# Optimization experiments

Measured on AMD Instinct MI355X. Metric: run time of the kernel, lower is better.

## Reference

```python
import jax, jax.numpy as jnp
import numpy as np

DIM = 1024
HID = 2816
E = 8
TOPK = 2
B, S = 4, 1024


def setup_inputs() -> dict:
    key = jax.random.key(0)
    k_x, k_g, k1, k2, k3 = jax.random.split(key, 5)
    scale_d = 1.0 / np.sqrt(DIM)
    scale_h = 1.0 / np.sqrt(HID)
    return {
        "x": jax.random.normal(k_x, (B, S, DIM), dtype=jnp.float32),
        "Wg": jax.random.normal(k_g, (E, DIM), dtype=jnp.float32) * scale_d,   # gate: Linear(dim, E), no bias
        "W1": jax.random.normal(k1, (E, HID, DIM), dtype=jnp.float32) * scale_d,  # swiglu gate proj
        "W3": jax.random.normal(k3, (E, HID, DIM), dtype=jnp.float32) * scale_d,  # swiglu up proj
        "W2": jax.random.normal(k2, (E, DIM, HID), dtype=jnp.float32) * scale_h,  # down proj
    }


def reference(x, Wg, W1, W3, W2):
    Bsz, Ssz, D = x.shape
    xt = x.reshape(Bsz * Ssz, D)                        # [T, D]

    # Gating: top-k over expert scores, softmax over selected logits
    scores = xt @ Wg.T                                   # [T, E]
    top_vals, top_idx = jax.lax.top_k(scores, TOPK)      # [T, K]
    weights = jax.nn.softmax(top_vals, axis=-1)          # [T, K]

    # Dense grouped SwiGLU: run every expert on every token (vectorized),
    # then gather the top-k expert outputs per token.
    h1 = jnp.einsum('td,ehd->teh', xt, W1)               # [T, E, H]
    h3 = jnp.einsum('td,ehd->teh', xt, W3)               # [T, E, H]
    expert_out = jnp.einsum('teh,edh->ted', jax.nn.silu(h1) * h3, W2)  # [T, E, D]

    # Gather per-token selected experts and combine with gate weights
    idx = top_idx[:, :, None]                            # [T, K, 1]
    sel = jnp.take_along_axis(expert_out, idx, axis=1)   # [T, K, D]
    out = jnp.sum(sel * weights[:, :, None], axis=1)     # [T, D]
    return out.reshape(Bsz, Ssz, D)
```

## Files before the change

kernel.cpp:

```cpp
#include <hip/hip_runtime.h>
#include <hip/hip_bf16.h>

#define DIM  1024
#define HID  2816
#define NE   8
#define NTOK 4096
#define NPAIR 8192
#define CAP  8192

typedef __bf16 bf16x8 __attribute__((ext_vector_type(8)));
typedef float f32x4 __attribute__((ext_vector_type(4)));

#define OFF_CNT  0
#define OFF_LIST 1024
#define OFF_WP   (OFF_LIST + NE*CAP*4)
#define OFF_H1   (OFF_WP + NPAIR*4)
#define OFF_XB   ((size_t)1 << 20)
#define OFF_W1B  ((size_t)10 << 20)
#define OFF_W3B  ((size_t)57 << 20)
#define OFF_H2   ((size_t)106 << 20)
#define WS_NEED  (OFF_H2 + (size_t)NPAIR * HID * 2)

#define GLB(p) ((const __attribute__((address_space(1))) void*)(p))
#define LDS(p) ((__attribute__((address_space(3))) void*)(p))

__global__ __launch_bounds__(64) void gate_kernel(
    const float* __restrict__ x, const float* __restrict__ Wg,
    int* __restrict__ counts, int* __restrict__ list, float* __restrict__ wpair) {
  int t = blockIdx.x;
  int lane = threadIdx.x;
  const float* xp = x + (size_t)t * DIM;
  float xr[16];
#pragma unroll
  for (int i = 0; i < 16; ++i) xr[i] = xp[lane + 64 * i];
  float s[NE];
#pragma unroll
  for (int e = 0; e < NE; ++e) {
    const float* wp = Wg + e * DIM;
    float acc = 0.f;
#pragma unroll
    for (int i = 0; i < 16; ++i) acc += xr[i] * wp[lane + 64 * i];
#pragma unroll
    for (int off = 32; off >= 1; off >>= 1) acc += __shfl_xor(acc, off, 64);
    s[e] = acc;
  }
  if (lane == 0) {
    int i0 = 0; float b0 = s[0];
#pragma unroll
    for (int e = 1; e < NE; ++e) if (s[e] > b0) { b0 = s[e]; i0 = e; }
    int i1 = -1; float b1 = -1e30f;
#pragma unroll
    for (int e = 0; e < NE; ++e) if (e != i0 && s[e] > b1) { b1 = s[e]; i1 = e; }
    float e1 = __expf(b1 - b0);
    float w0 = 1.f / (1.f + e1);
    float w1 = e1 * w0;
    int s0 = atomicAdd(&counts[i0], 1);
    list[i0 * CAP + s0] = 2 * t;
    wpair[2 * t] = w0;
    int s1 = atomicAdd(&counts[i1], 1);
    list[i1 * CAP + s1] = 2 * t + 1;
    wpair[2 * t + 1] = w1;
  }
}

__global__ __launch_bounds__(256) void cvt_kernel(
    const float* __restrict__ src, __bf16* __restrict__ dst) {
  size_t i = (((size_t)blockIdx.x * 256) + threadIdx.x) * 8;
  float4 f0 = *(const float4*)(src + i);
  float4 f1 = *(const float4*)(src + i + 4);
  bf16x8 v;
  v[0] = (__bf16)f0.x; v[1] = (__bf16)f0.y; v[2] = (__bf16)f0.z; v[3] = (__bf16)f0.w;
  v[4] = (__bf16)f1.x; v[5] = (__bf16)f1.y; v[6] = (__bf16)f1.z; v[7] = (__bf16)f1.w;
  *(bf16x8*)(dst + i) = v;
}


__global__ __launch_bounds__(256, 2) void up2_kernel(
    const __bf16* __restrict__ xb, const __bf16* __restrict__ w1b,
    const __bf16* __restrict__ w3b, const int* __restrict__ counts,
    const int* __restrict__ list, __bf16* __restrict__ Hbuf) {
  int e = blockIdx.z;
  int cnt = counts[e];
  int m0 = blockIdx.y * 128;
  if (m0 >= cnt) return;
  int h0 = blockIdx.x * 128;

  __shared__ __bf16 As[128 * 64];
  __shared__ __bf16 B1s[128 * 64];
  __shared__ __bf16 B3s[128 * 64];

  int tid = threadIdx.x;
  int lane = tid & 63;
  int w = tid >> 6;
  int cl = lane & 15, hi = lane >> 4;
  int wr = w >> 1, wc = w & 1;
  int l8 = lane >> 3, cc = lane & 7;

  const __bf16* asrc[4];
  const __bf16* b1src[4];
  const __bf16* b3src[4];
#pragma unroll
  for (int i = 0; i < 4; ++i) {
    int r = (w * 4 + i) * 8 + l8;
    int csel = (cc ^ (r & 7)) * 8;
    int mrow = m0 + r; if (mrow > cnt - 1) mrow = cnt - 1;
    int p = list[e * CAP + mrow];
    asrc[i]  = xb + (size_t)(p >> 1) * DIM + csel;
    b1src[i] = w1b + ((size_t)e * HID + h0 + r) * DIM + csel;
    b3src[i] = w3b + ((size_t)e * HID + h0 + r) * DIM + csel;
  }

  f32x4 acc1[4][4] = {};
  f32x4 acc3[4][4] = {};

  for (int k0 = 0; k0 < DIM; k0 += 64) {
#pragma unroll
    for (int i = 0; i < 4; ++i) {
      int q = (w * 4 + i) * 1024;
      __builtin_amdgcn_global_load_lds(GLB(asrc[i] + k0),  LDS((char*)As  + q), 16, 0, 0);
      __builtin_amdgcn_global_load_lds(GLB(b1src[i] + k0), LDS((char*)B1s + q), 16, 0, 0);
      __builtin_amdgcn_global_load_lds(GLB(b3src[i] + k0), LDS((char*)B3s + q), 16, 0, 0);
    }
    __syncthreads();
#pragma unroll
    for (int ks = 0; ks < 2; ++ks) {
      bf16x8 a[4], bb1[4], bb3[4];
#pragma unroll
      for (int mi = 0; mi < 4; ++mi) {
        int r = wr * 64 + mi * 16 + cl;
        int c = (hi + ks * 4) ^ (cl & 7);
        a[mi] = *(const bf16x8*)((const char*)As + r * 128 + c * 16);
      }
#pragma unroll
      for (int ni = 0; ni < 4; ++ni) {
        int r = wc * 64 + ni * 16 + cl;
        int c = (hi + ks * 4) ^ (cl & 7);
        bb1[ni] = *(const bf16x8*)((const char*)B1s + r * 128 + c * 16);
        bb3[ni] = *(const bf16x8*)((const char*)B3s + r * 128 + c * 16);
      }
#pragma unroll
      for (int mi = 0; mi < 4; ++mi)
#pragma unroll
        for (int ni = 0; ni < 4; ++ni) {
          acc1[mi][ni] = __builtin_amdgcn_mfma_f32_16x16x32_bf16(a[mi], bb1[ni], acc1[mi][ni], 0, 0, 0);
          acc3[mi][ni] = __builtin_amdgcn_mfma_f32_16x16x32_bf16(a[mi], bb3[ni], acc3[mi][ni], 0, 0, 0);
        }
    }
    __syncthreads();
  }

#pragma unroll
  for (int mi = 0; mi < 4; ++mi) {
#pragma unroll
    for (int rr = 0; rr < 4; ++rr) {
      int m = m0 + wr * 64 + mi * 16 + hi * 4 + rr;
      if (m < cnt) {
        int p = list[e * CAP + m];
        __bf16* hp = Hbuf + (size_t)p * HID + h0 + wc * 64 + cl;
#pragma unroll
        for (int ni = 0; ni < 4; ++ni) {
          float v1 = acc1[mi][ni][rr], v3 = acc3[mi][ni][rr];
          float g = (v1 / (1.f + __expf(-v1))) * v3;
          hp[ni * 16] = (__bf16)g;
        }
      }
    }
  }
}

__global__ __launch_bounds__(256, 2) void down2_kernel(
    const __bf16* __restrict__ Hbuf, const __bf16* __restrict__ w2b,
    const int* __restrict__ counts, const int* __restrict__ list,
    const float* __restrict__ wpair, float* __restrict__ out) {
  int e = blockIdx.z;
  int cnt = counts[e];
  int m0 = blockIdx.y * 128;
  if (m0 >= cnt) return;
  int d0 = blockIdx.x * 128;

  __shared__ __bf16 As[128 * 64];
  __shared__ __bf16 Bs[128 * 64];

  int tid = threadIdx.x;
  int lane = tid & 63;
  int w = tid >> 6;
  int cl = lane & 15, hi = lane >> 4;
  int wr = w >> 1, wc = w & 1;
  int l8 = lane >> 3, cc = lane & 7;

  const __bf16* asrc[4];
  const __bf16* bsrc[4];
#pragma unroll
  for (int i = 0; i < 4; ++i) {
    int r = (w * 4 + i) * 8 + l8;
    int csel = (cc ^ (r & 7)) * 8;
    int mrow = m0 + r; if (mrow > cnt - 1) mrow = cnt - 1;
    int p = list[e * CAP + mrow];
    asrc[i] = Hbuf + (size_t)p * HID + csel;
    bsrc[i] = w2b + ((size_t)e * DIM + d0 + r) * HID + csel;
  }

  f32x4 acc[4][4] = {};

  for (int k0 = 0; k0 < HID; k0 += 64) {
#pragma unroll
    for (int i = 0; i < 4; ++i) {
      int q = (w * 4 + i) * 1024;
      __builtin_amdgcn_global_load_lds(GLB(asrc[i] + k0), LDS((char*)As + q), 16, 0, 0);
      __builtin_amdgcn_global_load_lds(GLB(bsrc[i] + k0), LDS((char*)Bs + q), 16, 0, 0);
    }
    __syncthreads();
#pragma unroll
    for (int ks = 0; ks < 2; ++ks) {
      bf16x8 a[4], b[4];
#pragma unroll
      for (int mi = 0; mi < 4; ++mi) {
        int r = wr * 64 + mi * 16 + cl;
        int c = (hi + ks * 4) ^ (cl & 7);
        a[mi] = *(const bf16x8*)((const char*)As + r * 128 + c * 16);
      }
#pragma unroll
      for (int ni = 0; ni < 4; ++ni) {
        int r = wc * 64 + ni * 16 + cl;
        int c = (hi + ks * 4) ^ (cl & 7);
        b[ni] = *(const bf16x8*)((const char*)Bs + r * 128 + c * 16);
      }
#pragma unroll
      for (int mi = 0; mi < 4; ++mi)
#pragma unroll
        for (int ni = 0; ni < 4; ++ni)
          acc[mi][ni] = __builtin_amdgcn_mfma_f32_16x16x32_bf16(a[mi], b[ni], acc[mi][ni], 0, 0, 0);
    }
    __syncthreads();
  }

#pragma unroll
  for (int mi = 0; mi < 4; ++mi) {
#pragma unroll
    for (int rr = 0; rr < 4; ++rr) {
      int m = m0 + wr * 64 + mi * 16 + hi * 4 + rr;
      if (m < cnt) {
        int p = list[e * CAP + m];
        int t = p >> 1;
        float wgt = wpair[p];
        float* op = out + (size_t)t * DIM + d0 + wc * 64 + cl;
#pragma unroll
        for (int ni = 0; ni < 4; ++ni)
          atomicAdd(&op[ni * 16], wgt * acc[mi][ni][rr]);
      }
    }
  }
}

__device__ __forceinline__ void cvt_store16(__bf16* dst, const float* src) {
#pragma unroll
  for (int j = 0; j < 2; ++j) {
    float4 f0 = *(const float4*)(src + j * 8);
    float4 f1 = *(const float4*)(src + j * 8 + 4);
    bf16x8 v;
    v[0] = (__bf16)f0.x; v[1] = (__bf16)f0.y; v[2] = (__bf16)f0.z; v[3] = (__bf16)f0.w;
    v[4] = (__bf16)f1.x; v[5] = (__bf16)f1.y; v[6] = (__bf16)f1.z; v[7] = (__bf16)f1.w;
    *(bf16x8*)(dst + j * 8) = v;
  }
}

__global__ __launch_bounds__(256) void up_kernel(
    const float* __restrict__ x, const float* __restrict__ W1,
    const float* __restrict__ W3, const int* __restrict__ counts,
    const int* __restrict__ list, __bf16* __restrict__ Hbuf) {
  int e = blockIdx.z;
  int cnt = counts[e];
  int m0 = blockIdx.y * 64;
  if (m0 >= cnt) return;
  int h0 = blockIdx.x * 64;

  __shared__ __bf16 As[64][72];
  __shared__ __bf16 B1s[64][72];
  __shared__ __bf16 B3s[64][72];

  int tid = threadIdx.x;
  int r = tid >> 2;
  int cs = (tid & 3) * 16;

  const float* asrc = nullptr;
  int mrow = m0 + r;
  if (mrow < cnt) {
    int p = list[e * CAP + mrow];
    asrc = x + (size_t)(p >> 1) * DIM;
  }
  const float* b1src = W1 + ((size_t)e * HID + (h0 + r)) * DIM;
  const float* b3src = W3 + ((size_t)e * HID + (h0 + r)) * DIM;

  int lane = tid & 63;
  int w = tid >> 6;
  int wr = w >> 1, wc = w & 1;
  int cl = lane & 15, hi = lane >> 4;

  f32x4 acc1[2][2] = {};
  f32x4 acc3[2][2] = {};

  for (int k0 = 0; k0 < DIM; k0 += 64) {
    if (asrc) {
      cvt_store16(&As[r][cs], asrc + k0 + cs);
    } else {
      bf16x8 z = {};
      *(bf16x8*)&As[r][cs] = z;
      *(bf16x8*)&As[r][cs + 8] = z;
    }
    cvt_store16(&B1s[r][cs], b1src + k0 + cs);
    cvt_store16(&B3s[r][cs], b3src + k0 + cs);
    __syncthreads();
#pragma unroll
    for (int ks = 0; ks < 64; ks += 32) {
      bf16x8 a[2], b1f[2], b3f[2];
#pragma unroll
      for (int mi = 0; mi < 2; ++mi)
        a[mi] = *(const bf16x8*)&As[wr * 32 + mi * 16 + cl][ks + hi * 8];
#pragma unroll
      for (int ni = 0; ni < 2; ++ni) {
        b1f[ni] = *(const bf16x8*)&B1s[wc * 32 + ni * 16 + cl][ks + hi * 8];
        b3f[ni] = *(const bf16x8*)&B3s[wc * 32 + ni * 16 + cl][ks + hi * 8];
      }
#pragma unroll
      for (int mi = 0; mi < 2; ++mi)
#pragma unroll
        for (int ni = 0; ni < 2; ++ni) {
          acc1[mi][ni] = __builtin_amdgcn_mfma_f32_16x16x32_bf16(a[mi], b1f[ni], acc1[mi][ni], 0, 0, 0);
          acc3[mi][ni] = __builtin_amdgcn_mfma_f32_16x16x32_bf16(a[mi], b3f[ni], acc3[mi][ni], 0, 0, 0);
        }
    }
    __syncthreads();
  }

#pragma unroll
  for (int mi = 0; mi < 2; ++mi) {
#pragma unroll
    for (int rr = 0; rr < 4; ++rr) {
      int m = m0 + wr * 32 + mi * 16 + hi * 4 + rr;
      if (m < cnt) {
        int p = list[e * CAP + m];
        __bf16* hp = Hbuf + (size_t)p * HID + h0 + wc * 32 + cl;
#pragma unroll
        for (int ni = 0; ni < 2; ++ni) {
          float v1 = acc1[mi][ni][rr], v3 = acc3[mi][ni][rr];
          float g = (v1 / (1.f + __expf(-v1))) * v3;
          hp[ni * 16] = (__bf16)g;
        }
      }
    }
  }
}

__global__ __launch_bounds__(256) void down_kernel(
    const __bf16* __restrict__ Hbuf, const float* __restrict__ W2,
    const int* __restrict__ counts, const int* __restrict__ list,
    const float* __restrict__ wpair, float* __restrict__ out) {
  int e = blockIdx.z;
  int cnt = counts[e];
  int m0 = blockIdx.y * 64;
  if (m0 >= cnt) return;
  int d0 = blockIdx.x * 64;

  __shared__ __bf16 As[64][72];
  __shared__ __bf16 Bs[64][72];

  int tid = threadIdx.x;
  int r = tid >> 2;
  int cs = (tid & 3) * 16;

  const __bf16* asrc = nullptr;
  int mrow = m0 + r;
  if (mrow < cnt) {
    int p = list[e * CAP + mrow];
    asrc = Hbuf + (size_t)p * HID;
  }
  const float* bsrc = W2 + ((size_t)e * DIM + (d0 + r)) * HID;

  int lane = tid & 63;
  int w = tid >> 6;
  int wr = w >> 1, wc = w & 1;
  int cl = lane & 15, hi = lane >> 4;

  f32x4 acc[2][2] = {};

  for (int k0 = 0; k0 < HID; k0 += 64) {
    if (asrc) {
      *(bf16x8*)&As[r][cs]     = *(const bf16x8*)(asrc + k0 + cs);
      *(bf16x8*)&As[r][cs + 8] = *(const bf16x8*)(asrc + k0 + cs + 8);
    } else {
      bf16x8 z = {};
      *(bf16x8*)&As[r][cs] = z;
      *(bf16x8*)&As[r][cs + 8] = z;
    }
    cvt_store16(&Bs[r][cs], bsrc + k0 + cs);
    __syncthreads();
#pragma unroll
    for (int ks = 0; ks < 64; ks += 32) {
      bf16x8 a[2], b[2];
#pragma unroll
      for (int mi = 0; mi < 2; ++mi)
        a[mi] = *(const bf16x8*)&As[wr * 32 + mi * 16 + cl][ks + hi * 8];
#pragma unroll
      for (int ni = 0; ni < 2; ++ni)
        b[ni] = *(const bf16x8*)&Bs[wc * 32 + ni * 16 + cl][ks + hi * 8];
#pragma unroll
      for (int mi = 0; mi < 2; ++mi)
#pragma unroll
        for (int ni = 0; ni < 2; ++ni)
          acc[mi][ni] = __builtin_amdgcn_mfma_f32_16x16x32_bf16(a[mi], b[ni], acc[mi][ni], 0, 0, 0);
    }
    __syncthreads();
  }

#pragma unroll
  for (int mi = 0; mi < 2; ++mi) {
#pragma unroll
    for (int rr = 0; rr < 4; ++rr) {
      int m = m0 + wr * 32 + mi * 16 + hi * 4 + rr;
      if (m < cnt) {
        int p = list[e * CAP + m];
        int t = p >> 1;
        float wgt = wpair[p];
        float* op = out + (size_t)t * DIM + d0 + wc * 32 + cl;
#pragma unroll
        for (int ni = 0; ni < 2; ++ni)
          atomicAdd(&op[ni * 16], wgt * acc[mi][ni][rr]);
      }
    }
  }
}

extern "C" void kernel_launch(void* const* d_in, const int* in_sizes, int n_in,
                              void* d_out, int out_size, void* d_ws, size_t ws_size,
                              hipStream_t stream) {
  const float* x  = (const float*)d_in[0];
  const float* Wg = (const float*)d_in[1];
  const float* W1 = (const float*)d_in[2];
  const float* W3 = (const float*)d_in[3];
  const float* W2 = (const float*)d_in[4];
  float* out = (float*)d_out;

  char* ws = (char*)d_ws;
  int* counts  = (int*)(ws + OFF_CNT);
  int* list    = (int*)(ws + OFF_LIST);
  float* wpair = (float*)(ws + OFF_WP);

  hipMemsetAsync(counts, 0, 64, stream);
  hipMemsetAsync(d_out, 0, (size_t)out_size * sizeof(float), stream);

  gate_kernel<<<NTOK, 64, 0, stream>>>(x, Wg, counts, list, wpair);

  if (ws_size >= WS_NEED) {
    __bf16* xb   = (__bf16*)(ws + OFF_XB);
    __bf16* w1b  = (__bf16*)(ws + OFF_W1B);
    __bf16* w3b  = (__bf16*)(ws + OFF_W3B);
    __bf16* Hbuf = (__bf16*)(ws + OFF_H2);

    cvt_kernel<<<NTOK * DIM / 2048, 256, 0, stream>>>(x, xb);
    cvt_kernel<<<NE * HID * DIM / 2048, 256, 0, stream>>>(W1, w1b);
    cvt_kernel<<<NE * HID * DIM / 2048, 256, 0, stream>>>(W3, w3b);

    up2_kernel<<<dim3(HID / 128, CAP / 128, NE), 256, 0, stream>>>(
        xb, w1b, w3b, counts, list, Hbuf);

    cvt_kernel<<<NE * DIM * HID / 2048, 256, 0, stream>>>(W2, w1b);

    down2_kernel<<<dim3(DIM / 128, CAP / 128, NE), 256, 0, stream>>>(
        Hbuf, w1b, counts, list, wpair, out);
  } else {
    __bf16* Hbuf = (__bf16*)(ws + OFF_H1);
    up_kernel<<<dim3(HID / 64, CAP / 64, NE), 256, 0, stream>>>(x, W1, W3, counts, list, Hbuf);
    down_kernel<<<dim3(DIM / 64, CAP / 64, NE), 256, 0, stream>>>(Hbuf, W2, counts, list, wpair, out);
  }
}
```

Before: 399.2 us.

## Double-buffer MoE GEMMs, enlarge up tile, replace atomics with combine pass

The up-projection kernel now uses 512 threads with 256-row tiles and a single packed B buffer holding the W1 and W3 rows. It applies the gate weight in its SwiGLU epilogue. Both GEMM kernels gain double-buffered LDS staging so the next K tile loads while the current one computes. The down kernel writes per-pair bf16 outputs to a scratch buffer instead of doing float atomicAdds into the output, and a new combine kernel sums each token's two rows, which also removes the output memset. This trades atomic contention for an extra pass and bf16 rounding of the partial outputs, and relies on every token having exactly two pair slots.

```diff
diff --git a/kernel.cpp b/kernel.cpp
--- a/kernel.cpp
+++ b/kernel.cpp
@@ -75,92 +75,96 @@
 }
 
 
-__global__ __launch_bounds__(256, 2) void up2_kernel(
+__global__ __launch_bounds__(512, 2) void up3_kernel(
     const __bf16* __restrict__ xb, const __bf16* __restrict__ w1b,
     const __bf16* __restrict__ w3b, const int* __restrict__ counts,
-    const int* __restrict__ list, __bf16* __restrict__ Hbuf) {
+    const int* __restrict__ list, const float* __restrict__ wpair,
+    __bf16* __restrict__ Hbuf) {
   int e = blockIdx.z;
   int cnt = counts[e];
-  int m0 = blockIdx.y * 128;
+  int m0 = blockIdx.y * 256;
   if (m0 >= cnt) return;
   int h0 = blockIdx.x * 128;
 
-  __shared__ __bf16 As[128 * 64];
-  __shared__ __bf16 B1s[128 * 64];
-  __shared__ __bf16 B3s[128 * 64];
+  __shared__ __bf16 As[2][256 * 64];
+  __shared__ __bf16 Bs[2][256 * 64];
 
   int tid = threadIdx.x;
   int lane = tid & 63;
   int w = tid >> 6;
+  int wr = w >> 2, wc = w & 3;
   int cl = lane & 15, hi = lane >> 4;
-  int wr = w >> 1, wc = w & 1;
   int l8 = lane >> 3, cc = lane & 7;
 
   const __bf16* asrc[4];
-  const __bf16* b1src[4];
-  const __bf16* b3src[4];
+  const __bf16* bsrc[4];
 #pragma unroll
   for (int i = 0; i < 4; ++i) {
-    int r = (w * 4 + i) * 8 + l8;
+    int r = i * 64 + w * 8 + l8;
     int csel = (cc ^ (r & 7)) * 8;
     int mrow = m0 + r; if (mrow > cnt - 1) mrow = cnt - 1;
     int p = list[e * CAP + mrow];
-    asrc[i]  = xb + (size_t)(p >> 1) * DIM + csel;
-    b1src[i] = w1b + ((size_t)e * HID + h0 + r) * DIM + csel;
-    b3src[i] = w3b + ((size_t)e * HID + h0 + r) * DIM + csel;
-  }
-
-  f32x4 acc1[4][4] = {};
-  f32x4 acc3[4][4] = {};
-
-  for (int k0 = 0; k0 < DIM; k0 += 64) {
-#pragma unroll
-    for (int i = 0; i < 4; ++i) {
-      int q = (w * 4 + i) * 1024;
-      __builtin_amdgcn_global_load_lds(GLB(asrc[i] + k0),  LDS((char*)As  + q), 16, 0, 0);
-      __builtin_amdgcn_global_load_lds(GLB(b1src[i] + k0), LDS((char*)B1s + q), 16, 0, 0);
-      __builtin_amdgcn_global_load_lds(GLB(b3src[i] + k0), LDS((char*)B3s + q), 16, 0, 0);
-    }
-    __syncthreads();
-#pragma unroll
-    for (int ks = 0; ks < 2; ++ks) {
-      bf16x8 a[4], bb1[4], bb3[4];
-#pragma unroll
-      for (int mi = 0; mi < 4; ++mi) {
-        int r = wr * 64 + mi * 16 + cl;
-        int c = (hi + ks * 4) ^ (cl & 7);
-        a[mi] = *(const bf16x8*)((const char*)As + r * 128 + c * 16);
-      }
-#pragma unroll
-      for (int ni = 0; ni < 4; ++ni) {
-        int r = wc * 64 + ni * 16 + cl;
-        int c = (hi + ks * 4) ^ (cl & 7);
-        bb1[ni] = *(const bf16x8*)((const char*)B1s + r * 128 + c * 16);
-        bb3[ni] = *(const bf16x8*)((const char*)B3s + r * 128 + c * 16);
-      }
-#pragma unroll
-      for (int mi = 0; mi < 4; ++mi)
-#pragma unroll
-        for (int ni = 0; ni < 4; ++ni) {
-          acc1[mi][ni] = __builtin_amdgcn_mfma_f32_16x16x32_bf16(a[mi], bb1[ni], acc1[mi][ni], 0, 0, 0);
-          acc3[mi][ni] = __builtin_amdgcn_mfma_f32_16x16x32_bf16(a[mi], bb3[ni], acc3[mi][ni], 0, 0, 0);
-        }
-    }
-    __syncthreads();
-  }
-
-#pragma unroll
-  for (int mi = 0; mi < 4; ++mi) {
+    asrc[i] = xb + (size_t)(p >> 1) * DIM + csel;
+    bsrc[i] = (r < 128 ? w1b + ((size_t)e * HID + h0 + r) * DIM
+                       : w3b + ((size_t)e * HID + h0 + (r - 128)) * DIM) + csel;
+  }
+
+  f32x4 acc1[8][2] = {};
+  f32x4 acc3[8][2] = {};
+
+#define UP_STAGE(buf, k0)                                                          \
+  _Pragma("unroll") for (int i = 0; i < 4; ++i) {                                  \
+    int q = i * 8192 + w * 1024;                                                   \
+    __builtin_amdgcn_global_load_lds(GLB(asrc[i] + (k0)), LDS((char*)As[buf] + q), 16, 0, 0); \
+    __builtin_amdgcn_global_load_lds(GLB(bsrc[i] + (k0)), LDS((char*)Bs[buf] + q), 16, 0, 0); \
+  }
+
+#define UP_COMPUTE(buf)                                                            \
+  _Pragma("unroll") for (int ks = 0; ks < 2; ++ks) {                               \
+    int c = hi + ks * 4;                                                           \
+    bf16x8 a[8], b1[2], b3[2];                                                     \
+    _Pragma("unroll") for (int mi = 0; mi < 8; ++mi) {                             \
+      int r = wr * 128 + mi * 16 + cl;                                             \
+      a[mi] = *(const bf16x8*)((const char*)As[buf] + r * 128 + ((c ^ (r & 7)) * 16)); \
+    }                                                                              \
+    _Pragma("unroll") for (int ni = 0; ni < 2; ++ni) {                             \
+      int r1 = wc * 32 + ni * 16 + cl;                                             \
+      b1[ni] = *(const bf16x8*)((const char*)Bs[buf] + r1 * 128 + ((c ^ (r1 & 7)) * 16)); \
+      int r3 = 128 + r1;                                                           \
+      b3[ni] = *(const bf16x8*)((const char*)Bs[buf] + r3 * 128 + ((c ^ (r3 & 7)) * 16)); \
+    }                                                                              \
+    _Pragma("unroll") for (int mi = 0; mi < 8; ++mi)                               \
+      _Pragma("unroll") for (int ni = 0; ni < 2; ++ni) {                           \
+        acc1[mi][ni] = __builtin_amdgcn_mfma_f32_16x16x32_bf16(a[mi], b1[ni], acc1[mi][ni], 0, 0, 0); \
+        acc3[mi][ni] = __builtin_amdgcn_mfma_f32_16x16x32_bf16(a[mi], b3[ni], acc3[mi][ni], 0, 0, 0); \
+      }                                                                            \
+  }
+
+  UP_STAGE(0, 0);
+  __syncthreads();
+  int cur = 0;
+#pragma unroll 1
+  for (int kt = 0; kt < DIM / 64 - 1; ++kt) {
+    UP_STAGE(cur ^ 1, (kt + 1) * 64);
+    UP_COMPUTE(cur);
+    __syncthreads();
+    cur ^= 1;
+  }
+  UP_COMPUTE(cur);
+
+#pragma unroll
+  for (int mi = 0; mi < 8; ++mi) {
 #pragma unroll
     for (int rr = 0; rr < 4; ++rr) {
-      int m = m0 + wr * 64 + mi * 16 + hi * 4 + rr;
+      int m = m0 + wr * 128 + mi * 16 + hi * 4 + rr;
       if (m < cnt) {
         int p = list[e * CAP + m];
-        __bf16* hp = Hbuf + (size_t)p * HID + h0 + wc * 64 + cl;
-#pragma unroll
-        for (int ni = 0; ni < 4; ++ni) {
+        float wgt = wpair[p];
+        __bf16* hp = Hbuf + (size_t)p * HID + h0 + wc * 32 + cl;
+#pragma unroll
+        for (int ni = 0; ni < 2; ++ni) {
           float v1 = acc1[mi][ni][rr], v3 = acc3[mi][ni][rr];
-          float g = (v1 / (1.f + __expf(-v1))) * v3;
+          float g = (v1 / (1.f + __expf(-v1))) * v3 * wgt;
           hp[ni * 16] = (__bf16)g;
         }
       }
@@ -168,31 +172,31 @@
   }
 }
 
-__global__ __launch_bounds__(256, 2) void down2_kernel(
+__global__ __launch_bounds__(256, 2) void down3_kernel(
     const __bf16* __restrict__ Hbuf, const __bf16* __restrict__ w2b,
     const int* __restrict__ counts, const int* __restrict__ list,
-    const float* __restrict__ wpair, float* __restrict__ out) {
+    __bf16* __restrict__ Obuf) {
   int e = blockIdx.z;
   int cnt = counts[e];
   int m0 = blockIdx.y * 128;
   if (m0 >= cnt) return;
   int d0 = blockIdx.x * 128;
 
-  __shared__ __bf16 As[128 * 64];
-  __shared__ __bf16 Bs[128 * 64];
+  __shared__ __bf16 As[2][128 * 64];
+  __shared__ __bf16 Bs[2][128 * 64];
 
   int tid = threadIdx.x;
   int lane = tid & 63;
   int w = tid >> 6;
+  int wr = w >> 1, wc = w & 1;
   int cl = lane & 15, hi = lane >> 4;
-  int wr = w >> 1, wc = w & 1;
   int l8 = lane >> 3, cc = lane & 7;
 
   const __bf16* asrc[4];
   const __bf16* bsrc[4];
 #pragma unroll
   for (int i = 0; i < 4; ++i) {
-    int r = (w * 4 + i) * 8 + l8;
+    int r = i * 32 + w * 8 + l8;
     int csel = (cc ^ (r & 7)) * 8;
     int mrow = m0 + r; if (mrow > cnt - 1) mrow = cnt - 1;
     int p = list[e * CAP + mrow];
@@ -202,37 +206,41 @@
 
   f32x4 acc[4][4] = {};
 
-  for (int k0 = 0; k0 < HID; k0 += 64) {
-#pragma unroll
-    for (int i = 0; i < 4; ++i) {
-      int q = (w * 4 + i) * 1024;
-      __builtin_amdgcn_global_load_lds(GLB(asrc[i] + k0), LDS((char*)As + q), 16, 0, 0);
-      __builtin_amdgcn_global_load_lds(GLB(bsrc[i] + k0), LDS((char*)Bs + q), 16, 0, 0);
-    }
-    __syncthreads();
-#pragma unroll
-    for (int ks = 0; ks < 2; ++ks) {
-      bf16x8 a[4], b[4];
-#pragma unroll
-      for (int mi = 0; mi < 4; ++mi) {
-        int r = wr * 64 + mi * 16 + cl;
-        int c = (hi + ks * 4) ^ (cl & 7);
-        a[mi] = *(const bf16x8*)((const char*)As + r * 128 + c * 16);
-      }
-#pragma unroll
-      for (int ni = 0; ni < 4; ++ni) {
-        int r = wc * 64 + ni * 16 + cl;
-        int c = (hi + ks * 4) ^ (cl & 7);
-        b[ni] = *(const bf16x8*)((const char*)Bs + r * 128 + c * 16);
-      }
-#pragma unroll
-      for (int mi = 0; mi < 4; ++mi)
-#pragma unroll
-        for (int ni = 0; ni < 4; ++ni)
-          acc[mi][ni] = __builtin_amdgcn_mfma_f32_16x16x32_bf16(a[mi], b[ni], acc[mi][ni], 0, 0, 0);
-    }
-    __syncthreads();
-  }
+#define DN_STAGE(buf, k0)                                                          \
+  _Pragma("unroll") for (int i = 0; i < 4; ++i) {                                  \
+    int q = i * 4096 + w * 1024;                                                   \
+    __builtin_amdgcn_global_load_lds(GLB(asrc[i] + (k0)), LDS((char*)As[buf] + q), 16, 0, 0); \
+    __builtin_amdgcn_global_load_lds(GLB(bsrc[i] + (k0)), LDS((char*)Bs[buf] + q), 16, 0, 0); \
+  }
+
+#define DN_COMPUTE(buf)                                                            \
+  _Pragma("unroll") for (int ks = 0; ks < 2; ++ks) {                               \
+    int c = hi + ks * 4;                                                           \
+    bf16x8 a[4], b[4];                                                             \
+    _Pragma("unroll") for (int mi = 0; mi < 4; ++mi) {                             \
+      int r = wr * 64 + mi * 16 + cl;                                              \
+      a[mi] = *(const bf16x8*)((const char*)As[buf] + r * 128 + ((c ^ (r & 7)) * 16)); \
+    }                                                                              \
+    _Pragma("unroll") for (int ni = 0; ni < 4; ++ni) {                             \
+      int r = wc * 64 + ni * 16 + cl;                                              \
+      b[ni] = *(const bf16x8*)((const char*)Bs[buf] + r * 128 + ((c ^ (r & 7)) * 16)); \
+    }                                                                              \
+    _Pragma("unroll") for (int mi = 0; mi < 4; ++mi)                               \
+      _Pragma("unroll") for (int ni = 0; ni < 4; ++ni)                             \
+        acc[mi][ni] = __builtin_amdgcn_mfma_f32_16x16x32_bf16(a[mi], b[ni], acc[mi][ni], 0, 0, 0); \
+  }
+
+  DN_STAGE(0, 0);
+  __syncthreads();
+  int cur = 0;
+#pragma unroll 1
+  for (int kt = 0; kt < HID / 64 - 1; ++kt) {
+    DN_STAGE(cur ^ 1, (kt + 1) * 64);
+    DN_COMPUTE(cur);
+    __syncthreads();
+    cur ^= 1;
+  }
+  DN_COMPUTE(cur);
 
 #pragma unroll
   for (int mi = 0; mi < 4; ++mi) {
@@ -241,15 +249,28 @@
       int m = m0 + wr * 64 + mi * 16 + hi * 4 + rr;
       if (m < cnt) {
         int p = list[e * CAP + m];
-        int t = p >> 1;
-        float wgt = wpair[p];
-        float* op = out + (size_t)t * DIM + d0 + wc * 64 + cl;
+        __bf16* op = Obuf + (size_t)p * DIM + d0 + wc * 64 + cl;
 #pragma unroll
         for (int ni = 0; ni < 4; ++ni)
-          atomicAdd(&op[ni * 16], wgt * acc[mi][ni][rr]);
+          op[ni * 16] = (__bf16)acc[mi][ni][rr];
       }
     }
   }
+}
+
+__global__ __launch_bounds__(256) void combine_kernel(
+    const __bf16* __restrict__ Obuf, float* __restrict__ out) {
+  size_t j = (((size_t)blockIdx.x * 256) + threadIdx.x) * 8;
+  size_t t = j >> 10;
+  bf16x8 a = *(const bf16x8*)(Obuf + j + t * DIM);
+  bf16x8 b = *(const bf16x8*)(Obuf + j + t * DIM + DIM);
+  float4 o0, o1;
+  o0.x = (float)a[0] + (float)b[0]; o0.y = (float)a[1] + (float)b[1];
+  o0.z = (float)a[2] + (float)b[2]; o0.w = (float)a[3] + (float)b[3];
+  o1.x = (float)a[4] + (float)b[4]; o1.y = (float)a[5] + (float)b[5];
+  o1.z = (float)a[6] + (float)b[6]; o1.w = (float)a[7] + (float)b[7];
+  *(float4*)(out + j) = o0;
+  *(float4*)(out + j + 4) = o1;
 }
 
 __device__ __forceinline__ void cvt_store16(__bf16* dst, const float* src) {
@@ -446,7 +467,6 @@
   float* wpair = (float*)(ws + OFF_WP);
 
   hipMemsetAsync(counts, 0, 64, stream);
-  hipMemsetAsync(d_out, 0, (size_t)out_size * sizeof(float), stream);
 
   gate_kernel<<<NTOK, 64, 0, stream>>>(x, Wg, counts, list, wpair);
 
@@ -455,19 +475,23 @@
     __bf16* w1b  = (__bf16*)(ws + OFF_W1B);
     __bf16* w3b  = (__bf16*)(ws + OFF_W3B);
     __bf16* Hbuf = (__bf16*)(ws + OFF_H2);
+    __bf16* Obuf = (__bf16*)(ws + OFF_W3B);
 
     cvt_kernel<<<NTOK * DIM / 2048, 256, 0, stream>>>(x, xb);
     cvt_kernel<<<NE * HID * DIM / 2048, 256, 0, stream>>>(W1, w1b);
     cvt_kernel<<<NE * HID * DIM / 2048, 256, 0, stream>>>(W3, w3b);
 
-    up2_kernel<<<dim3(HID / 128, CAP / 128, NE), 256, 0, stream>>>(
-        xb, w1b, w3b, counts, list, Hbuf);
+    up3_kernel<<<dim3(HID / 128, CAP / 256, NE), 512, 0, stream>>>(
+        xb, w1b, w3b, counts, list, wpair, Hbuf);
 
     cvt_kernel<<<NE * DIM * HID / 2048, 256, 0, stream>>>(W2, w1b);
 
-    down2_kernel<<<dim3(DIM / 128, CAP / 128, NE), 256, 0, stream>>>(
-        Hbuf, w1b, counts, list, wpair, out);
+    down3_kernel<<<dim3(DIM / 128, CAP / 128, NE), 256, 0, stream>>>(
+        Hbuf, w1b, counts, list, Obuf);
+
+    combine_kernel<<<NTOK * DIM / 2048, 256, 0, stream>>>(Obuf, out);
   } else {
+    hipMemsetAsync(d_out, 0, (size_t)out_size * sizeof(float), stream);
     __bf16* Hbuf = (__bf16*)(ws + OFF_H1);
     up_kernel<<<dim3(HID / 64, CAP / 64, NE), 256, 0, stream>>>(x, W1, W3, counts, list, Hbuf);
     down_kernel<<<dim3(DIM / 64, CAP / 64, NE), 256, 0, stream>>>(Hbuf, W2, counts, list, wpair, out);
```

Result: slower. 457.9 us (+14.7%).

## Replace atomic scatter with per-pair bf16 output buffer and combine kernel

Applied to the files above, without the earlier changes.

The down-projection now writes each token-expert pair's result to a bf16 buffer instead of doing fp32 atomicAdds into the output, and a new combine kernel sums the two pairs per token. The gate weight is folded into the up-projection epilogue, the x-to-bf16 conversion is fused into the gate kernel, and the output memset is dropped on the fast path. Both GEMMs use a flattened 1D grid with an expert-interleaving block remap. The aim is to remove atomic contention and extra launches, at the cost of another bf16 rounding on the output and an extra pass over the pair buffer.

```diff
diff --git a/kernel.cpp b/kernel.cpp
--- a/kernel.cpp
+++ b/kernel.cpp
@@ -7,6 +7,12 @@
 #define NTOK 4096
 #define NPAIR 8192
 #define CAP  8192
+
+#define NT_UP (HID / 128)
+#define MT    (CAP / 128)
+#define NT_DN (DIM / 128)
+#define NWG_UP (NE * NT_UP * MT)
+#define NWG_DN (NE * NT_DN * MT)
 
 typedef __bf16 bf16x8 __attribute__((ext_vector_type(8)));
 typedef float f32x4 __attribute__((ext_vector_type(4)));
@@ -26,13 +32,19 @@
 
 __global__ __launch_bounds__(64) void gate_kernel(
     const float* __restrict__ x, const float* __restrict__ Wg,
-    int* __restrict__ counts, int* __restrict__ list, float* __restrict__ wpair) {
+    int* __restrict__ counts, int* __restrict__ list, float* __restrict__ wpair,
+    __bf16* __restrict__ xb) {
   int t = blockIdx.x;
   int lane = threadIdx.x;
   const float* xp = x + (size_t)t * DIM;
   float xr[16];
 #pragma unroll
   for (int i = 0; i < 16; ++i) xr[i] = xp[lane + 64 * i];
+  if (xb) {
+    __bf16* xo = xb + (size_t)t * DIM;
+#pragma unroll
+    for (int i = 0; i < 16; ++i) xo[lane + 64 * i] = (__bf16)xr[i];
+  }
   float s[NE];
 #pragma unroll
   for (int e = 0; e < NE; ++e) {
@@ -75,15 +87,19 @@
 }
 
 
-__global__ __launch_bounds__(256, 2) void up2_kernel(
+__global__ __launch_bounds__(256, 2) void up4_kernel(
     const __bf16* __restrict__ xb, const __bf16* __restrict__ w1b,
     const __bf16* __restrict__ w3b, const int* __restrict__ counts,
-    const int* __restrict__ list, __bf16* __restrict__ Hbuf) {
-  int e = blockIdx.z;
+    const int* __restrict__ list, const float* __restrict__ wpair,
+    __bf16* __restrict__ Hbuf) {
+  int bid = blockIdx.x;
+  int g = (bid & 7) * (NWG_UP / 8) + (bid >> 3);
+  int e = g / (NT_UP * MT);
+  int rr0 = g % (NT_UP * MT);
   int cnt = counts[e];
-  int m0 = blockIdx.y * 128;
+  int m0 = (rr0 % MT) * 128;
   if (m0 >= cnt) return;
-  int h0 = blockIdx.x * 128;
+  int h0 = (rr0 / MT) * 128;
 
   __shared__ __bf16 As[128 * 64];
   __shared__ __bf16 B1s[128 * 64];
@@ -124,19 +140,18 @@
     __syncthreads();
 #pragma unroll
     for (int ks = 0; ks < 2; ++ks) {
+      int c = hi + ks * 4;
       bf16x8 a[4], bb1[4], bb3[4];
 #pragma unroll
       for (int mi = 0; mi < 4; ++mi) {
         int r = wr * 64 + mi * 16 + cl;
-        int c = (hi + ks * 4) ^ (cl & 7);
-        a[mi] = *(const bf16x8*)((const char*)As + r * 128 + c * 16);
+        a[mi] = *(const bf16x8*)((const char*)As + r * 128 + ((c ^ (r & 7)) * 16));
       }
 #pragma unroll
       for (int ni = 0; ni < 4; ++ni) {
         int r = wc * 64 + ni * 16 + cl;
-        int c = (hi + ks * 4) ^ (cl & 7);
-        bb1[ni] = *(const bf16x8*)((const char*)B1s + r * 128 + c * 16);
-        bb3[ni] = *(const bf16x8*)((const char*)B3s + r * 128 + c * 16);
+        bb1[ni] = *(const bf16x8*)((const char*)B1s + r * 128 + ((c ^ (r & 7)) * 16));
+        bb3[ni] = *(const bf16x8*)((const char*)B3s + r * 128 + ((c ^ (r & 7)) * 16));
       }
 #pragma unroll
       for (int mi = 0; mi < 4; ++mi)
@@ -156,27 +171,31 @@
       int m = m0 + wr * 64 + mi * 16 + hi * 4 + rr;
       if (m < cnt) {
         int p = list[e * CAP + m];
+        float wgt = wpair[p];
         __bf16* hp = Hbuf + (size_t)p * HID + h0 + wc * 64 + cl;
 #pragma unroll
         for (int ni = 0; ni < 4; ++ni) {
           float v1 = acc1[mi][ni][rr], v3 = acc3[mi][ni][rr];
-          float g = (v1 / (1.f + __expf(-v1))) * v3;
-          hp[ni * 16] = (__bf16)g;
+          float gv = (v1 / (1.f + __expf(-v1))) * v3 * wgt;
+          hp[ni * 16] = (__bf16)gv;
         }
       }
     }
   }
 }
 
-__global__ __launch_bounds__(256, 2) void down2_kernel(
+__global__ __launch_bounds__(256, 2) void down4_kernel(
     const __bf16* __restrict__ Hbuf, const __bf16* __restrict__ w2b,
     const int* __restrict__ counts, const int* __restrict__ list,
-    const float* __restrict__ wpair, float* __restrict__ out) {
-  int e = blockIdx.z;
+    __bf16* __restrict__ Obuf) {
+  int bid = blockIdx.x;
+  int g = (bid & 7) * (NWG_DN / 8) + (bid >> 3);
+  int e = g / (NT_DN * MT);
+  int rr0 = g % (NT_DN * MT);
   int cnt = counts[e];
-  int m0 = blockIdx.y * 128;
+  int m0 = (rr0 % MT) * 128;
   if (m0 >= cnt) return;
-  int d0 = blockIdx.x * 128;
+  int d0 = (rr0 / MT) * 128;
 
   __shared__ __bf16 As[128 * 64];
   __shared__ __bf16 Bs[128 * 64];
@@ -212,18 +231,17 @@
     __syncthreads();
 #pragma unroll
     for (int ks = 0; ks < 2; ++ks) {
+      int c = hi + ks * 4;
       bf16x8 a[4], b[4];
 #pragma unroll
       for (int mi = 0; mi < 4; ++mi) {
         int r = wr * 64 + mi * 16 + cl;
-        int c = (hi + ks * 4) ^ (cl & 7);
-        a[mi] = *(const bf16x8*)((const char*)As + r * 128 + c * 16);
+        a[mi] = *(const bf16x8*)((const char*)As + r * 128 + ((c ^ (r & 7)) * 16));
       }
 #pragma unroll
       for (int ni = 0; ni < 4; ++ni) {
         int r = wc * 64 + ni * 16 + cl;
-        int c = (hi + ks * 4) ^ (cl & 7);
-        b[ni] = *(const bf16x8*)((const char*)Bs + r * 128 + c * 16);
+        b[ni] = *(const bf16x8*)((const char*)Bs + r * 128 + ((c ^ (r & 7)) * 16));
       }
 #pragma unroll
       for (int mi = 0; mi < 4; ++mi)
@@ -241,15 +259,28 @@
       int m = m0 + wr * 64 + mi * 16 + hi * 4 + rr;
       if (m < cnt) {
         int p = list[e * CAP + m];
-        int t = p >> 1;
-        float wgt = wpair[p];
-        float* op = out + (size_t)t * DIM + d0 + wc * 64 + cl;
+        __bf16* op = Obuf + (size_t)p * DIM + d0 + wc * 64 + cl;
 #pragma unroll
         for (int ni = 0; ni < 4; ++ni)
-          atomicAdd(&op[ni * 16], wgt * acc[mi][ni][rr]);
-      }
-    }
-  }
+          op[ni * 16] = (__bf16)acc[mi][ni][rr];
+      }
+    }
+  }
+}
+
+__global__ __launch_bounds__(256) void combine_kernel(
+    const __bf16* __restrict__ Obuf, float* __restrict__ out) {
+  size_t j = (((size_t)blockIdx.x * 256) + threadIdx.x) * 8;
+  size_t t = j >> 10;
+  bf16x8 a = *(const bf16x8*)(Obuf + j + t * DIM);
+  bf16x8 b = *(const bf16x8*)(Obuf + j + t * DIM + DIM);
+  float4 o0, o1;
+  o0.x = (float)a[0] + (float)b[0]; o0.y = (float)a[1] + (float)b[1];
+  o0.z = (float)a[2] + (float)b[2]; o0.w = (float)a[3] + (float)b[3];
+  o1.x = (float)a[4] + (float)b[4]; o1.y = (float)a[5] + (float)b[5];
+  o1.z = (float)a[6] + (float)b[6]; o1.w = (float)a[7] + (float)b[7];
+  *(float4*)(out + j) = o0;
+  *(float4*)(out + j + 4) = o1;
 }
 
 __device__ __forceinline__ void cvt_store16(__bf16* dst, const float* src) {
@@ -343,8 +374,8 @@
 #pragma unroll
         for (int ni = 0; ni < 2; ++ni) {
           float v1 = acc1[mi][ni][rr], v3 = acc3[mi][ni][rr];
-          float g = (v1 / (1.f + __expf(-v1))) * v3;
-          hp[ni * 16] = (__bf16)g;
+          float gg = (v1 / (1.f + __expf(-v1))) * v3;
+          hp[ni * 16] = (__bf16)gg;
         }
       }
     }
@@ -446,29 +477,30 @@
   float* wpair = (float*)(ws + OFF_WP);
 
   hipMemsetAsync(counts, 0, 64, stream);
-  hipMemsetAsync(d_out, 0, (size_t)out_size * sizeof(float), stream);
-
-  gate_kernel<<<NTOK, 64, 0, stream>>>(x, Wg, counts, list, wpair);
 
   if (ws_size >= WS_NEED) {
     __bf16* xb   = (__bf16*)(ws + OFF_XB);
     __bf16* w1b  = (__bf16*)(ws + OFF_W1B);
     __bf16* w3b  = (__bf16*)(ws + OFF_W3B);
     __bf16* Hbuf = (__bf16*)(ws + OFF_H2);
-
-    cvt_kernel<<<NTOK * DIM / 2048, 256, 0, stream>>>(x, xb);
+    __bf16* Obuf = (__bf16*)(ws + OFF_W3B);
+
+    gate_kernel<<<NTOK, 64, 0, stream>>>(x, Wg, counts, list, wpair, xb);
+
     cvt_kernel<<<NE * HID * DIM / 2048, 256, 0, stream>>>(W1, w1b);
     cvt_kernel<<<NE * HID * DIM / 2048, 256, 0, stream>>>(W3, w3b);
 
-    up2_kernel<<<dim3(HID / 128, CAP / 128, NE), 256, 0, stream>>>(
-        xb, w1b, w3b, counts, list, Hbuf);
+    up4_kernel<<<NWG_UP, 256, 0, stream>>>(xb, w1b, w3b, counts, list, wpair, Hbuf);
 
     cvt_kernel<<<NE * DIM * HID / 2048, 256, 0, stream>>>(W2, w1b);
 
-    down2_kernel<<<dim3(DIM / 128, CAP / 128, NE), 256, 0, stream>>>(
-        Hbuf, w1b, counts, list, wpair, out);
+    down4_kernel<<<NWG_DN, 256, 0, stream>>>(Hbuf, w1b, counts, list, Obuf);
+
+    combine_kernel<<<NTOK * DIM / 2048, 256, 0, stream>>>(Obuf, out);
   } else {
+    hipMemsetAsync(d_out, 0, (size_t)out_size * sizeof(float), stream);
     __bf16* Hbuf = (__bf16*)(ws + OFF_H1);
+    gate_kernel<<<NTOK, 64, 0, stream>>>(x, Wg, counts, list, wpair, nullptr);
     up_kernel<<<dim3(HID / 64, CAP / 64, NE), 256, 0, stream>>>(x, W1, W3, counts, list, Hbuf);
     down_kernel<<<dim3(DIM / 64, CAP / 64, NE), 256, 0, stream>>>(Hbuf, W2, counts, list, wpair, out);
   }
```

Result: faster. 391.3 us (-2.0%).
